# Kernel tuning notes

Hardware: AMD Instinct MI355X
Metric: run time of the kernel (lower is better)

Reference implementation:

```python
import jax, jax.numpy as jnp
import numpy as np

N, E = 50000, 800000
FIN, CLUS, FOU1, FOU2, HLIN, OUTP = 5, 256, 128, 256, 256, 10


def setup_inputs():
    key = jax.random.key(0)
    ks = jax.random.split(key, 16)
    p = lambda k, shape: jax.random.normal(k, shape, jnp.float32) * 0.05
    return {
        "x": jax.random.normal(ks[0], (N, FIN), jnp.float32),
        "edge_index": jax.random.randint(ks[1], (2, E), 0, N),
        "edge_wht": jax.random.uniform(ks[2], (E,), jnp.float32),
        "W1p": p(ks[3], (FIN, CLUS)), "R1p": p(ks[4], (FIN, CLUS)), "b1p": jnp.zeros((CLUS,), jnp.float32),
        "W1e": p(ks[5], (FIN, FOU1)), "R1e": p(ks[6], (FIN, FOU1)), "b1e": jnp.zeros((FOU1,), jnp.float32),
        "W2p": p(ks[7], (FOU1, 1)), "R2p": p(ks[8], (FOU1, 1)), "b2p": jnp.zeros((1,), jnp.float32),
        "W2e": p(ks[9], (FOU1, FOU2)), "R2e": p(ks[10], (FOU1, FOU2)), "b2e": jnp.zeros((FOU2,), jnp.float32),
        "Wl1": p(ks[11], (FOU2, HLIN)), "bl1": jnp.zeros((HLIN,), jnp.float32),
        "Wl2": p(ks[12], (HLIN, OUTP)), "bl2": jnp.zeros((OUTP,), jnp.float32),
    }


def _forward(x, edge_index, edge_wht, W1p, R1p, b1p, W1e, R1e, b1e,
             W2p, R2p, b2p, W2e, R2e, b2e, Wl1, bl1, Wl2, bl2):
    n = x.shape[0]
    src, dst = edge_index[0], edge_index[1]  # A[src, dst] = w
    cnt = jax.ops.segment_sum(jnp.ones_like(edge_wht), dst, num_segments=n)
    denom = jnp.maximum(cnt, 1.0)[:, None]

    def spline_conv_k1(h, W, R, b):
        # SplineConv, kernel_size=1: B-spline basis collapses to a single kernel
        # weight -> out_i = mean_{j->i}(h_j @ W) + h_i @ R + b (pseudo coords inert)
        agg = jax.ops.segment_sum((h @ W)[src], dst, num_segments=n) / denom
        return agg + h @ R + b

    mat_s = spline_conv_k1(x, W1p, R1p, b1p)               # [N, CLUS]
    mat_y = jax.nn.relu(spline_conv_k1(x, W1e, R1e, b1e))  # [N, FOU1]

    S = jax.nn.softmax(mat_s, axis=-1)                     # [N, CLUS]
    pooled = S.T @ mat_y                                   # [CLUS, FOU1]

    # laplacian regularizer: trace(S^T L S)/N with L = I - D^-1/2 A D^-1/2
    deg = jax.ops.segment_sum(edge_wht, src, num_segments=n)
    d_is = jnp.where(deg > 0, jax.lax.rsqrt(jnp.maximum(deg, 1e-30)), 0.0)
    asn = d_is[:, None] * jax.ops.segment_sum(
        (edge_wht * d_is[dst])[:, None] * S[dst], src, num_segments=n)
    diag_mask = (deg > 0).astype(S.dtype)
    reg1 = (jnp.sum(diag_mask[:, None] * S * S) - jnp.sum(S * asn)) / n

    # Pooled graph: S^T A S is fully dense positive, so nonzero() gives the
    # complete graph -> mean aggregation over incoming edges = global node mean.
    mean_h = jnp.mean(pooled, axis=0, keepdims=True)       # [1, FOU1]
    s2 = mean_h @ W2p + pooled @ R2p + b2p                 # [CLUS, 1]
    y2 = jax.nn.relu(mean_h @ W2e + pooled @ R2e + b2e)    # [CLUS, FOU2]
    S2 = jax.nn.softmax(s2, axis=-1)                       # identically ones
    g = S2.T @ y2                                          # [1, FOU2]

    h1 = jax.nn.relu(g @ Wl1 + bl1)
    logits = h1 @ Wl2 + bl2
    return jax.nn.log_softmax(logits[0], axis=-1)[None], reg1


def reference(x, edge_index, edge_wht, W1p, R1p, b1p, W1e, R1e, b1e,
              W2p, R2p, b2p, W2e, R2e, b2e, Wl1, bl1, Wl2, bl2):
    return _forward(x, edge_index, edge_wht, W1p, R1p, b1p, W1e, R1e, b1e,
                    W2p, R2p, b2p, W2e, R2e, b2e, Wl1, bl1, Wl2, bl2)
```

## Files before the change

### kernel.cpp

```cpp
#include <hip/hip_runtime.h>
#include <hip/hip_bf16.h>
#include <hip/hip_fp16.h>


#define PR 256
#define NBMAX 256
#define SCH 2048

typedef _Float16 f16x8 __attribute__((ext_vector_type(8)));
typedef float f32x4 __attribute__((ext_vector_type(4)));

__device__ inline int udot8(uint32_t a, uint32_t b, int c) {
#if __has_builtin(__builtin_amdgcn_udot8)
    return __builtin_amdgcn_udot8(a, b, c, false);
#else
    #pragma unroll
    for (int i = 0; i < 8; i++)
        c += (int)((a >> (4 * i)) & 15) * (int)((b >> (4 * i)) & 15);
    return c;
#endif
}

__launch_bounds__(1024)
__global__ void k_hist(const int* __restrict__ ei, uint32_t* __restrict__ keys,
                       int* __restrict__ hd, int* __restrict__ hs, int E) {
    __shared__ int lhd[NBMAX], lhs[NBMAX];
    int t = threadIdx.x;
    if (t < NBMAX) { lhd[t] = 0; lhs[t] = 0; }
    __syncthreads();
    int idx = blockIdx.x * blockDim.x + t;
    int stride = gridDim.x * blockDim.x;
    for (int e = idx; e < E; e += stride) {
        uint32_t s = (uint32_t)ei[e];
        uint32_t d = (uint32_t)ei[E + e];
        keys[e] = (s << 16) | d;
        atomicAdd(&lhd[d >> 8], 1);
        atomicAdd(&lhs[s >> 8], 1);
    }
    __syncthreads();
    if (t < NBMAX) {
        if (lhd[t]) atomicAdd(&hd[t], lhd[t]);
        if (lhs[t]) atomicAdd(&hs[t], lhs[t]);
    }
}

__launch_bounds__(NBMAX)
__global__ void k_prefix(const int* __restrict__ hd, const int* __restrict__ hs,
                         int* __restrict__ offd, int* __restrict__ offs,
                         int* __restrict__ cd, int* __restrict__ cs, int NB) {
    __shared__ int sd[NBMAX], ss[NBMAX];
    int t = threadIdx.x;
    sd[t] = (t < NB) ? hd[t] : 0;
    ss[t] = (t < NB) ? hs[t] : 0;
    __syncthreads();
    #pragma unroll
    for (int o = 1; o < NBMAX; o <<= 1) {
        int vd = (t >= o) ? sd[t - o] : 0;
        int vs = (t >= o) ? ss[t - o] : 0;
        __syncthreads();
        sd[t] += vd; ss[t] += vs;
        __syncthreads();
    }
    int ed = (t == 0) ? 0 : sd[t - 1];
    int es = (t == 0) ? 0 : ss[t - 1];
    if (t < NB) { offd[t] = ed; cd[t] = ed; offs[t] = es; cs[t] = es; }
    if (t == NB - 1) { offd[NB] = sd[t]; offs[NB] = ss[t]; }
}

__launch_bounds__(1024)
__global__ void k_scatter(const uint32_t* __restrict__ keys, const float* __restrict__ ew,
                          int* __restrict__ cd, int* __restrict__ cs,
                          uint32_t* __restrict__ bd, float* __restrict__ bwd,
                          uint32_t* __restrict__ bs, int E, int NB) {
    __shared__ int lhd[NBMAX], lhs[NBMAX];
    __shared__ int bD[NBMAX], bS[NBMAX];
    int t = threadIdx.x;
    int e0 = blockIdx.x * SCH;
    int e1 = min(e0 + SCH, E);
    if (t < NBMAX) { lhd[t] = 0; lhs[t] = 0; }
    __syncthreads();
    for (int e = e0 + t; e < e1; e += 1024) {
        uint32_t k = keys[e];
        atomicAdd(&lhd[(k >> 8) & 0xff], 1);
        atomicAdd(&lhs[k >> 24], 1);
    }
    __syncthreads();
    if (t < NB) {
        bD[t] = lhd[t] ? atomicAdd(&cd[t], lhd[t]) : 0;
        bS[t] = lhs[t] ? atomicAdd(&cs[t], lhs[t]) : 0;
        lhd[t] = 0; lhs[t] = 0;
    }
    __syncthreads();
    for (int e = e0 + t; e < e1; e += 1024) {
        uint32_t k = keys[e];
        float w = ew[e];
        int db = (k >> 8) & 0xff;
        int sb = k >> 24;
        int rd = atomicAdd(&lhd[db], 1);
        bd[bD[db] + rd] = k;
        bwd[bD[db] + rd] = w;
        int rs = atomicAdd(&lhs[sb], 1);
        __half hw = __float2half(w);
        bs[bS[sb] + rs] = ((uint32_t)*(uint16_t*)&hw << 16) | ((k >> 16) & 0xffu);
    }
}

__launch_bounds__(1024)
__global__ void k_consume(const uint32_t* __restrict__ bd, const uint32_t* __restrict__ bs,
                          const int* __restrict__ offd, const int* __restrict__ offs,
                          const float* __restrict__ x, float* __restrict__ ninfo, int N) {
    __shared__ float accx[PR][6];
    __shared__ float accd[PR];
    int t = threadIdx.x;
    int b = blockIdx.x;
    int base = b * PR;
    uint32_t pr = (uint32_t)min(PR, N - base);

    for (int k = t; k < PR * 6; k += 1024) (&accx[0][0])[k] = 0.f;
    for (int k = t; k < PR; k += 1024) accd[k] = 0.f;
    __syncthreads();

    int r0 = offd[b], r1 = offd[b + 1];
    for (int r = r0 + t; r < r1; r += 1024) {
        uint32_t k = bd[r];
        uint32_t src = k >> 16;
        uint32_t dl = k & 0xffu;
        const float* xp = x + (size_t)src * 5;
        atomicAdd(&accx[dl][0], xp[0]);
        atomicAdd(&accx[dl][1], xp[1]);
        atomicAdd(&accx[dl][2], xp[2]);
        atomicAdd(&accx[dl][3], xp[3]);
        atomicAdd(&accx[dl][4], xp[4]);
        atomicAdd(&accx[dl][5], 1.0f);
    }
    int s0 = offs[b], s1 = offs[b + 1];
    for (int r = s0 + t; r < s1; r += 1024) {
        uint32_t k = bs[r];
        uint16_t hw = (uint16_t)(k >> 16);
        atomicAdd(&accd[k & 0xffu], __half2float(*(__half*)&hw));
    }
    __syncthreads();

    for (uint32_t n = t; n < pr; n += 1024) {
        float dg = accd[n];
        float dis = (dg > 0.f) ? rsqrtf(fmaxf(dg, 1e-30f)) : 0.f;
        float* o = ninfo + (size_t)(base + n) * 8;
        *(float4*)(o + 0) = make_float4(accx[n][0], accx[n][1], accx[n][2], accx[n][3]);
        *(float4*)(o + 4) = make_float4(accx[n][4], accx[n][5], dg, dis);
    }
}

#define STRD 40
__launch_bounds__(1024)
__global__ void k_node(const float* __restrict__ x,
                       const float* __restrict__ ninfo,
                       const float* __restrict__ W1p, const float* __restrict__ R1p,
                       const float* __restrict__ b1p,
                       const float* __restrict__ W1e, const float* __restrict__ R1e,
                       const float* __restrict__ b1e,
                       uint32_t* __restrict__ Sq, float* __restrict__ csc,
                       uint32_t* __restrict__ parts,
                       float* __restrict__ scal, int N) {
    __shared__ __half St[256 * STRD];
    __shared__ __half Yt[128 * STRD];
    __shared__ float Wc[10][256];
    __shared__ float bc[256];
    __shared__ float We[10][128];
    __shared__ float be[128];
    __shared__ float red[16];

    int t = threadIdx.x;
    int wv = t >> 6, lane = t & 63;
    int nl = t >> 5, sub = t & 31;

    for (int k = t; k < 2560; k += 1024) Wc[k >> 8][k & 255] = (k < 1280) ? W1p[k] : R1p[k - 1280];
    for (int k = t; k < 1280; k += 1024) We[k >> 7][k & 127] = (k < 640) ? W1e[k] : R1e[k - 640];
    if (t < 256) bc[t] = b1p[t];
    if (t < 128) be[t] = b1e[t];
    __syncthreads();

    f32x4 acc[8];
    #pragma unroll
    for (int ft = 0; ft < 8; ft++) acc[ft] = (f32x4){0.f, 0.f, 0.f, 0.f};
    float ssq = 0.f;

    int ntiles = (N + 31) >> 5;
    for (int tile = blockIdx.x; tile < ntiles; tile += (int)gridDim.x) {
        int i = tile * 32 + nl;
        if (i < N) {
            const float4* ni = (const float4*)(ninfo + (size_t)i * 8);
            float4 plo = ni[0];
            float4 phi = ni[1];
            float dg = phi.z;
            float dis = phi.w;
            float inv_dn = 1.0f / fmaxf(phi.y, 1.0f);
            float z[10];
            z[0] = plo.x * inv_dn; z[1] = plo.y * inv_dn; z[2] = plo.z * inv_dn;
            z[3] = plo.w * inv_dn; z[4] = phi.x * inv_dn;
            const float* xp = x + (size_t)i * 5;
            z[5] = xp[0]; z[6] = xp[1]; z[7] = xp[2]; z[8] = xp[3]; z[9] = xp[4];
            float m[8];
            #pragma unroll
            for (int j = 0; j < 8; j++) {
                int c = sub + 32 * j;
                float v = bc[c];
                #pragma unroll
                for (int d = 0; d < 10; d++) v += z[d] * Wc[d][c];
                m[j] = v;
            }
            float mx = m[0];
            #pragma unroll
            for (int j = 1; j < 8; j++) mx = fmaxf(mx, m[j]);
            #pragma unroll
            for (int o = 16; o > 0; o >>= 1) mx = fmaxf(mx, __shfl_xor(mx, o));
            float ls = 0.f;
            #pragma unroll
            for (int j = 0; j < 8; j++) { m[j] = __expf(m[j] - mx); ls += m[j]; }
            #pragma unroll
            for (int o = 16; o > 0; o >>= 1) ls += __shfl_xor(ls, o);
            float inv_l = 1.0f / ls;
            uint32_t qp = 0;
            #pragma unroll
            for (int j = 0; j < 8; j++) {
                int q = __float2int_rn(m[j] * 15.f);
                qp |= (uint32_t)min(q, 15) << (4 * j);
            }
            Sq[(size_t)i * 32 + sub] = qp;
            if (sub == 0) csc[i] = dis * inv_l * (1.0f / 15.0f);
            float sq = 0.f;
            #pragma unroll
            for (int j = 0; j < 8; j++) {
                float s = m[j] * inv_l;
                m[j] = s;
                sq += s * s;
                St[(sub + 32 * j) * STRD + nl] = __float2half(s);
            }
            if (dg > 0.f) ssq += sq;
            #pragma unroll
            for (int j = 0; j < 4; j++) {
                int f = sub + 32 * j;
                float v = be[f];
                #pragma unroll
                for (int d = 0; d < 10; d++) v += z[d] * We[d][f];
                Yt[f * STRD + nl] = __float2half(fmaxf(v, 0.f));
            }
        } else {
            #pragma unroll
            for (int j = 0; j < 8; j++) St[(sub + 32 * j) * STRD + nl] = __half(0.f);
            #pragma unroll
            for (int j = 0; j < 4; j++) Yt[(sub + 32 * j) * STRD + nl] = __half(0.f);
        }
        __syncthreads();
        {
            int r = lane & 15, kc = lane >> 4;
            uint4 au = *(const uint4*)&St[(wv * 16 + r) * STRD + kc * 8];
            f16x8 a = __builtin_bit_cast(f16x8, au);
            #pragma unroll
            for (int ft = 0; ft < 8; ft++) {
                uint4 bu = *(const uint4*)&Yt[(ft * 16 + r) * STRD + kc * 8];
                f16x8 b = __builtin_bit_cast(f16x8, bu);
                acc[ft] = __builtin_amdgcn_mfma_f32_16x16x32_f16(a, b, acc[ft], 0, 0, 0);
            }
        }
        __syncthreads();
    }

    {
        uint32_t* pw = parts + (size_t)blockIdx.x * 16384 + wv * 1024 + lane;
        #pragma unroll
        for (int ft = 0; ft < 8; ft++) {
            __hip_bfloat162 h0, h1;
            h0.x = __float2bfloat16(acc[ft][0]);
            h0.y = __float2bfloat16(acc[ft][1]);
            h1.x = __float2bfloat16(acc[ft][2]);
            h1.y = __float2bfloat16(acc[ft][3]);
            pw[(ft * 2) * 64]     = *(uint32_t*)&h0;
            pw[(ft * 2 + 1) * 64] = *(uint32_t*)&h1;
        }
    }

    #pragma unroll
    for (int o = 32; o > 0; o >>= 1) ssq += __shfl_xor(ssq, o);
    if (lane == 0) red[wv] = ssq;
    __syncthreads();
    if (t == 0) {
        float s = 0.f;
        #pragma unroll
        for (int w2 = 0; w2 < 16; w2++) s += red[w2];
        atomicAdd(&scal[0], s);
    }
}

__global__ void k_reduce(const uint32_t* __restrict__ parts,
                         float* __restrict__ pooled, int nparts) {
    int w = blockIdx.x * blockDim.x + threadIdx.x;
    float s0 = 0.f, s1 = 0.f;
    #pragma unroll 4
    for (int q = 0; q < nparts; q++) {
        uint32_t v = parts[(size_t)q * 16384 + w];
        __hip_bfloat162 h = *(__hip_bfloat162*)&v;
        s0 += __bfloat162float(h.x);
        s1 += __bfloat162float(h.y);
    }
    int lane = w & 63, idx = (w >> 6) & 15, wv = w >> 10;
    int ft = idx >> 1, h = idx & 1;
    int c = wv * 16 + ((lane >> 4) & 3) * 4 + 2 * h;
    int f = ft * 16 + (lane & 15);
    pooled[c * 128 + f] = s0;
    pooled[(c + 1) * 128 + f] = s1;
}

__launch_bounds__(256)
__global__ void k_edge_reg(const uint32_t* __restrict__ bd, const float* __restrict__ bwd,
                           const uint32_t* __restrict__ Sq, const float* __restrict__ csc,
                           float* __restrict__ scal, int E) {
    __shared__ float red[4];
    int t = threadIdx.x;
    int lane = t & 63;
    int sub = lane & 3;
    int grp = lane >> 2;
    int wv = t >> 6;
    int gw = blockIdx.x * (blockDim.x >> 6) + wv;
    int nwaves = gridDim.x * (blockDim.x >> 6);

    float acc = 0.f;
    for (int base = gw * 16; base < E; base += nwaves * 16) {
        int e = base + grp;
        int idot = 0;
        float sc = 0.f;
        if (e < E) {
            uint32_t k = bd[e];
            int s = (int)(k >> 16);
            int d = (int)(k & 0xffffu);
            const uint4* pa = (const uint4*)(Sq + (size_t)s * 32) + sub * 2;
            const uint4* pb = (const uint4*)(Sq + (size_t)d * 32) + sub * 2;
            uint4 A0 = pa[0], A1 = pa[1];
            uint4 B0 = pb[0], B1 = pb[1];
            idot = udot8(A0.x, B0.x, idot);
            idot = udot8(A0.y, B0.y, idot);
            idot = udot8(A0.z, B0.z, idot);
            idot = udot8(A0.w, B0.w, idot);
            idot = udot8(A1.x, B1.x, idot);
            idot = udot8(A1.y, B1.y, idot);
            idot = udot8(A1.z, B1.z, idot);
            idot = udot8(A1.w, B1.w, idot);
            sc = bwd[e] * csc[s] * csc[d];
        }
        #pragma unroll
        for (int o = 2; o > 0; o >>= 1) idot += __shfl_xor(idot, o);
        if (sub == 0) acc += sc * (float)idot;
    }

    #pragma unroll
    for (int o = 32; o > 0; o >>= 1) acc += __shfl_xor(acc, o);
    if (lane == 0) red[wv] = acc;
    __syncthreads();
    if (t == 0) atomicAdd(&scal[1], red[0] + red[1] + red[2] + red[3]);
}

__launch_bounds__(256)
__global__ void k_pool2(const float* __restrict__ pooled,
                        const float* __restrict__ W2e, const float* __restrict__ R2e,
                        const float* __restrict__ b2e, float* __restrict__ g) {
    __shared__ float mh[128];
    __shared__ float prow[128];
    int t = threadIdx.x;
    int c = blockIdx.x;
    if (t < 128) {
        float s = 0.f;
        for (int cc = 0; cc < 256; cc++) s += pooled[cc * 128 + t];
        mh[t] = s * (1.0f / 256.0f);
        prow[t] = pooled[c * 128 + t];
    }
    __syncthreads();
    float v = b2e[t];
    for (int k = 0; k < 128; k++)
        v += mh[k] * W2e[k * 256 + t] + prow[k] * R2e[k * 256 + t];
    v = fmaxf(v, 0.f);
    atomicAdd(&g[t], v);
}

__launch_bounds__(256)
__global__ void k_final(const float* __restrict__ g,
                        const float* __restrict__ Wl1, const float* __restrict__ bl1,
                        const float* __restrict__ Wl2, const float* __restrict__ bl2,
                        const float* __restrict__ scal, float* __restrict__ out, int N) {
    __shared__ float gs[256];
    __shared__ float h1[256];
    __shared__ float lg[10];
    int t = threadIdx.x;
    gs[t] = g[t];
    __syncthreads();
    float v = bl1[t];
    for (int k = 0; k < 256; k++) v += gs[k] * Wl1[k * 256 + t];
    h1[t] = fmaxf(v, 0.f);
    __syncthreads();
    if (t < 10) {
        float s = bl2[t];
        for (int k = 0; k < 256; k++) s += h1[k] * Wl2[k * 10 + t];
        lg[t] = s;
    }
    __syncthreads();
    if (t == 0) {
        float mx = lg[0];
        for (int j = 1; j < 10; j++) mx = fmaxf(mx, lg[j]);
        float ls = 0.f;
        for (int j = 0; j < 10; j++) ls += __expf(lg[j] - mx);
        float lse = mx + logf(ls);
        for (int j = 0; j < 10; j++) out[j] = lg[j] - lse;
        out[10] = (scal[0] - scal[1]) / (float)N;
    }
}

extern "C" void kernel_launch(void* const* d_in, const int* in_sizes, int n_in,
                              void* d_out, int out_size, void* d_ws, size_t ws_size,
                              hipStream_t stream) {
    const float* x   = (const float*)d_in[0];
    const int*   ei  = (const int*)d_in[1];
    const float* ew  = (const float*)d_in[2];
    const float* W1p = (const float*)d_in[3];
    const float* R1p = (const float*)d_in[4];
    const float* b1p = (const float*)d_in[5];
    const float* W1e = (const float*)d_in[6];
    const float* R1e = (const float*)d_in[7];
    const float* b1e = (const float*)d_in[8];
    const float* W2e = (const float*)d_in[12];
    const float* R2e = (const float*)d_in[13];
    const float* b2e = (const float*)d_in[14];
    const float* Wl1 = (const float*)d_in[15];
    const float* bl1 = (const float*)d_in[16];
    const float* Wl2 = (const float*)d_in[17];
    const float* bl2 = (const float*)d_in[18];
    float* out = (float*)d_out;

    int N = in_sizes[0] / 5;
    int E = in_sizes[1] / 2;
    int NB = (N + PR - 1) / PR;

    uint32_t* ws = (uint32_t*)d_ws;
    size_t off = 0;
    float* g    = (float*)(ws + off); off += 256;
    float* scal = (float*)(ws + off); off += 2;
    int* hd = (int*)(ws + off); off += NBMAX;
    int* hs = (int*)(ws + off); off += NBMAX;
    size_t zero_words = off;
    int* offd = (int*)(ws + off); off += NBMAX + 1;
    int* offs = (int*)(ws + off); off += NBMAX + 1;
    int* cd   = (int*)(ws + off); off += NBMAX;
    int* cs   = (int*)(ws + off); off += NBMAX;
    off = (off + 3) & ~(size_t)3;
    float* ninfo = (float*)(ws + off); off += (size_t)N * 8;
    float* csc   = (float*)(ws + off); off += (size_t)N;
    uint32_t* keys = ws + off; off += (size_t)E;
    uint32_t* bd   = ws + off; off += (size_t)E;
    float*    bwd  = (float*)(ws + off); off += (size_t)E;
    uint32_t* bs   = ws + off; off += (size_t)E;
    off = (off + 3) & ~(size_t)3;
    uint32_t* Sq = ws + off; off += (size_t)N * 32;
    float* pooled = (float*)(ws + off); off += 32768;
    size_t avail = (ws_size / 4 > off) ? (ws_size / 4 - off) : 0;
    int nparts = (int)(avail / 16384);
    if (nparts > 256) nparts = 256;
    if (nparts < 1) nparts = 1;
    uint32_t* parts = ws + off;

    hipMemsetAsync(d_ws, 0, zero_words * 4, stream);

    k_hist<<<104, 1024, 0, stream>>>(ei, keys, hd, hs, E);
    k_prefix<<<1, NBMAX, 0, stream>>>(hd, hs, offd, offs, cd, cs, NB);
    k_scatter<<<(E + SCH - 1) / SCH, 1024, 0, stream>>>(keys, ew, cd, cs, bd, bwd, bs, E, NB);
    k_consume<<<NB, 1024, 0, stream>>>(bd, bs, offd, offs, x, ninfo, N);
    k_node<<<nparts, 1024, 0, stream>>>(x, ninfo, W1p, R1p, b1p,
                                        W1e, R1e, b1e, Sq, csc, parts, scal, N);
    k_reduce<<<64, 256, 0, stream>>>(parts, pooled, nparts);
    k_edge_reg<<<2048, 256, 0, stream>>>(bd, bwd, Sq, csc, scal, E);
    k_pool2<<<256, 256, 0, stream>>>(pooled, W2e, R2e, b2e, g);
    k_final<<<1, 256, 0, stream>>>(g, Wl1, bl1, Wl2, bl2, scal, out, N);
}
```

Measured before the change: 220.6 us.

## Interleave edge key/weight records, double-buffer node tiles, retune edge-reg lane split

```diff
diff --git a/kernel.cpp b/kernel.cpp
--- a/kernel.cpp
+++ b/kernel.cpp
@@ -70,8 +70,8 @@
 __launch_bounds__(1024)
 __global__ void k_scatter(const uint32_t* __restrict__ keys, const float* __restrict__ ew,
                           int* __restrict__ cd, int* __restrict__ cs,
-                          uint32_t* __restrict__ bd, float* __restrict__ bwd,
-                          uint32_t* __restrict__ bs, int E, int NB) {
+                          uint2* __restrict__ bdw, uint32_t* __restrict__ bs,
+                          int E, int NB) {
     __shared__ int lhd[NBMAX], lhs[NBMAX];
     __shared__ int bD[NBMAX], bS[NBMAX];
     int t = threadIdx.x;
@@ -97,8 +97,10 @@
         int db = (k >> 8) & 0xff;
         int sb = k >> 24;
         int rd = atomicAdd(&lhd[db], 1);
-        bd[bD[db] + rd] = k;
-        bwd[bD[db] + rd] = w;
+        uint2 rec;
+        rec.x = k;
+        rec.y = __float_as_uint(w);
+        bdw[bD[db] + rd] = rec;
         int rs = atomicAdd(&lhs[sb], 1);
         __half hw = __float2half(w);
         bs[bS[sb] + rs] = ((uint32_t)*(uint16_t*)&hw << 16) | ((k >> 16) & 0xffu);
@@ -106,7 +108,7 @@
 }
 
 __launch_bounds__(1024)
-__global__ void k_consume(const uint32_t* __restrict__ bd, const uint32_t* __restrict__ bs,
+__global__ void k_consume(const uint2* __restrict__ bdw, const uint32_t* __restrict__ bs,
                           const int* __restrict__ offd, const int* __restrict__ offs,
                           const float* __restrict__ x, float* __restrict__ ninfo, int N) {
     __shared__ float accx[PR][6];
@@ -122,7 +124,7 @@
 
     int r0 = offd[b], r1 = offd[b + 1];
     for (int r = r0 + t; r < r1; r += 1024) {
-        uint32_t k = bd[r];
+        uint32_t k = bdw[r].x;
         uint32_t src = k >> 16;
         uint32_t dl = k & 0xffu;
         const float* xp = x + (size_t)src * 5;
@@ -151,7 +153,7 @@
 }
 
 #define STRD 40
-__launch_bounds__(1024)
+__launch_bounds__(1024, 8)
 __global__ void k_node(const float* __restrict__ x,
                        const float* __restrict__ ninfo,
                        const float* __restrict__ W1p, const float* __restrict__ R1p,
@@ -161,8 +163,8 @@
                        uint32_t* __restrict__ Sq, float* __restrict__ csc,
                        uint32_t* __restrict__ parts,
                        float* __restrict__ scal, int N) {
-    __shared__ __half St[256 * STRD];
-    __shared__ __half Yt[128 * STRD];
+    __shared__ __half St[2][256 * STRD];
+    __shared__ __half Yt[2][128 * STRD];
     __shared__ float Wc[10][256];
     __shared__ float bc[256];
     __shared__ float We[10][128];
@@ -183,6 +185,7 @@
     #pragma unroll
     for (int ft = 0; ft < 8; ft++) acc[ft] = (f32x4){0.f, 0.f, 0.f, 0.f};
     float ssq = 0.f;
+    int p = 0;
 
     int ntiles = (N + 31) >> 5;
     for (int tile = blockIdx.x; tile < ntiles; tile += (int)gridDim.x) {
@@ -233,7 +236,7 @@
                 float s = m[j] * inv_l;
                 m[j] = s;
                 sq += s * s;
-                St[(sub + 32 * j) * STRD + nl] = __float2half(s);
+                St[p][(sub + 32 * j) * STRD + nl] = __float2half(s);
             }
             if (dg > 0.f) ssq += sq;
             #pragma unroll
@@ -242,27 +245,27 @@
                 float v = be[f];
                 #pragma unroll
                 for (int d = 0; d < 10; d++) v += z[d] * We[d][f];
-                Yt[f * STRD + nl] = __float2half(fmaxf(v, 0.f));
+                Yt[p][f * STRD + nl] = __float2half(fmaxf(v, 0.f));
             }
         } else {
             #pragma unroll
-            for (int j = 0; j < 8; j++) St[(sub + 32 * j) * STRD + nl] = __half(0.f);
-            #pragma unroll
-            for (int j = 0; j < 4; j++) Yt[(sub + 32 * j) * STRD + nl] = __half(0.f);
+            for (int j = 0; j < 8; j++) St[p][(sub + 32 * j) * STRD + nl] = __half(0.f);
+            #pragma unroll
+            for (int j = 0; j < 4; j++) Yt[p][(sub + 32 * j) * STRD + nl] = __half(0.f);
         }
         __syncthreads();
         {
             int r = lane & 15, kc = lane >> 4;
-            uint4 au = *(const uint4*)&St[(wv * 16 + r) * STRD + kc * 8];
+            uint4 au = *(const uint4*)&St[p][(wv * 16 + r) * STRD + kc * 8];
             f16x8 a = __builtin_bit_cast(f16x8, au);
             #pragma unroll
             for (int ft = 0; ft < 8; ft++) {
-                uint4 bu = *(const uint4*)&Yt[(ft * 16 + r) * STRD + kc * 8];
+                uint4 bu = *(const uint4*)&Yt[p][(ft * 16 + r) * STRD + kc * 8];
                 f16x8 b = __builtin_bit_cast(f16x8, bu);
                 acc[ft] = __builtin_amdgcn_mfma_f32_16x16x32_f16(a, b, acc[ft], 0, 0, 0);
             }
         }
-        __syncthreads();
+        p ^= 1;
     }
 
     {
@@ -311,43 +314,45 @@
 }
 
 __launch_bounds__(256)
-__global__ void k_edge_reg(const uint32_t* __restrict__ bd, const float* __restrict__ bwd,
+__global__ void k_edge_reg(const uint2* __restrict__ bdw,
                            const uint32_t* __restrict__ Sq, const float* __restrict__ csc,
                            float* __restrict__ scal, int E) {
     __shared__ float red[4];
     int t = threadIdx.x;
     int lane = t & 63;
-    int sub = lane & 3;
-    int grp = lane >> 2;
+    int sub = lane & 1;
+    int grp = lane >> 1;
     int wv = t >> 6;
-    int gw = blockIdx.x * (blockDim.x >> 6) + wv;
-    int nwaves = gridDim.x * (blockDim.x >> 6);
+    int nblocks = (int)gridDim.x;
+    int bid = (int)blockIdx.x;
+    int swz = (bid & 7) * (nblocks >> 3) + (bid >> 3);
+    int gw = swz * (blockDim.x >> 6) + wv;
+    int nwaves = nblocks * (blockDim.x >> 6);
 
     float acc = 0.f;
-    for (int base = gw * 16; base < E; base += nwaves * 16) {
+    for (int base = gw * 32; base < E; base += nwaves * 32) {
         int e = base + grp;
         int idot = 0;
         float sc = 0.f;
         if (e < E) {
-            uint32_t k = bd[e];
+            uint2 rec = bdw[e];
+            uint32_t k = rec.x;
             int s = (int)(k >> 16);
             int d = (int)(k & 0xffffu);
-            const uint4* pa = (const uint4*)(Sq + (size_t)s * 32) + sub * 2;
-            const uint4* pb = (const uint4*)(Sq + (size_t)d * 32) + sub * 2;
-            uint4 A0 = pa[0], A1 = pa[1];
-            uint4 B0 = pb[0], B1 = pb[1];
-            idot = udot8(A0.x, B0.x, idot);
-            idot = udot8(A0.y, B0.y, idot);
-            idot = udot8(A0.z, B0.z, idot);
-            idot = udot8(A0.w, B0.w, idot);
-            idot = udot8(A1.x, B1.x, idot);
-            idot = udot8(A1.y, B1.y, idot);
-            idot = udot8(A1.z, B1.z, idot);
-            idot = udot8(A1.w, B1.w, idot);
-            sc = bwd[e] * csc[s] * csc[d];
+            const uint4* pa = (const uint4*)(Sq + (size_t)s * 32) + sub * 4;
+            const uint4* pb = (const uint4*)(Sq + (size_t)d * 32) + sub * 4;
+            #pragma unroll
+            for (int q = 0; q < 4; q++) {
+                uint4 A = pa[q];
+                uint4 B = pb[q];
+                idot = udot8(A.x, B.x, idot);
+                idot = udot8(A.y, B.y, idot);
+                idot = udot8(A.z, B.z, idot);
+                idot = udot8(A.w, B.w, idot);
+            }
+            sc = __uint_as_float(rec.y) * csc[s] * csc[d];
         }
-        #pragma unroll
-        for (int o = 2; o > 0; o >>= 1) idot += __shfl_xor(idot, o);
+        idot += __shfl_xor(idot, 1);
         if (sub == 0) acc += sc * (float)idot;
     }
 
@@ -452,15 +457,15 @@
     float* ninfo = (float*)(ws + off); off += (size_t)N * 8;
     float* csc   = (float*)(ws + off); off += (size_t)N;
     uint32_t* keys = ws + off; off += (size_t)E;
-    uint32_t* bd   = ws + off; off += (size_t)E;
-    float*    bwd  = (float*)(ws + off); off += (size_t)E;
-    uint32_t* bs   = ws + off; off += (size_t)E;
+    off = (off + 1) & ~(size_t)1;
+    uint2* bdw = (uint2*)(ws + off); off += (size_t)E * 2;
+    uint32_t* bs = ws + off; off += (size_t)E;
     off = (off + 3) & ~(size_t)3;
     uint32_t* Sq = ws + off; off += (size_t)N * 32;
     float* pooled = (float*)(ws + off); off += 32768;
     size_t avail = (ws_size / 4 > off) ? (ws_size / 4 - off) : 0;
     int nparts = (int)(avail / 16384);
-    if (nparts > 256) nparts = 256;
+    if (nparts > 512) nparts = 512;
     if (nparts < 1) nparts = 1;
     uint32_t* parts = ws + off;
 
@@ -468,12 +473,12 @@
 
     k_hist<<<104, 1024, 0, stream>>>(ei, keys, hd, hs, E);
     k_prefix<<<1, NBMAX, 0, stream>>>(hd, hs, offd, offs, cd, cs, NB);
-    k_scatter<<<(E + SCH - 1) / SCH, 1024, 0, stream>>>(keys, ew, cd, cs, bd, bwd, bs, E, NB);
-    k_consume<<<NB, 1024, 0, stream>>>(bd, bs, offd, offs, x, ninfo, N);
+    k_scatter<<<(E + SCH - 1) / SCH, 1024, 0, stream>>>(keys, ew, cd, cs, bdw, bs, E, NB);
+    k_consume<<<NB, 1024, 0, stream>>>(bdw, bs, offd, offs, x, ninfo, N);
     k_node<<<nparts, 1024, 0, stream>>>(x, ninfo, W1p, R1p, b1p,
                                         W1e, R1e, b1e, Sq, csc, parts, scal, N);
     k_reduce<<<64, 256, 0, stream>>>(parts, pooled, nparts);
-    k_edge_reg<<<2048, 256, 0, stream>>>(bd, bwd, Sq, csc, scal, E);
+    k_edge_reg<<<2048, 256, 0, stream>>>(bdw, Sq, csc, scal, E);
     k_pool2<<<256, 256, 0, stream>>>(pooled, W2e, R2e, b2e, g);
     k_final<<<1, 256, 0, stream>>>(g, Wl1, bl1, Wl2, bl2, scal, out, N);
 }
```

After: 283.4 us. 1.28x slower.
